# Performance work log

Measured on AMD Instinct MI355X. Metric: run time of the kernel, lower is better.

Reference implementation:

```python
import jax, jax.numpy as jnp
import numpy as np

B, P, E, D, A = 128, 49, 2048, 512, 512


def setup_inputs() -> dict:
    key = jax.random.key(0)
    ks = jax.random.split(key, 10)
    s = lambda k, shape, fan: jax.random.normal(k, shape, jnp.float32) * (1.0 / np.sqrt(fan))
    return {
        "encoder_out": jax.random.normal(ks[0], (B, P, E), jnp.float32),
        "decoder_hidden": jax.random.normal(ks[1], (B, D), jnp.float32),
        "We": s(ks[2], (A, E), E),  # encoder_att weight
        "be": jnp.zeros((A,), jnp.float32),
        "Wd": s(ks[3], (A, D), D),  # decoder_att weight
        "bd": jnp.zeros((A,), jnp.float32),
        "Wb": s(ks[4], (A, A, A), A),  # Bilinear weight [out,in1,in2]
        "bb": jnp.zeros((A,), jnp.float32),
        "Wf": s(ks[5], (1, A), A),  # full_att weight
        "bf": jnp.zeros((1,), jnp.float32),
    }


def reference(encoder_out, decoder_hidden, We, be, Wd, bd, Wb, bb, Wf, bf):
    # att1: [B,P,A]; att2: [B,A]
    att1 = jnp.einsum('bpe,ae->bpa', encoder_out, We) + be
    att2 = jnp.einsum('bd,ad->ba', decoder_hidden, Wd) + bd
    # nn.Bilinear(att1, att2_expanded): out[b,p,k] = sum_ij att1[b,p,i]*Wb[k,i,j]*att2[b,j] + bb[k]
    # contract att2 first since it is shared across the P=49 positions
    u = jnp.einsum('bj,kij->bki', att2, Wb)            # [B,A,A]
    bil = jnp.einsum('bpi,bki->bpk', att1, u) + bb     # [B,P,A]
    att = jnp.einsum('bpk,ok->bpo', jax.nn.relu(bil), Wf)[..., 0] + bf[0]  # [B,P]
    alpha = jax.nn.softmax(att, axis=1)                # [B,P]
    attention_weighted_encoding = jnp.einsum('bpe,bp->be', encoder_out, alpha)
    return (attention_weighted_encoding, alpha)
```

## Files before the change

### kernel.cpp

```cpp
#include <hip/hip_runtime.h>
#include <stdint.h>

typedef unsigned short ushort_t;
typedef float f32x4 __attribute__((ext_vector_type(4)));
typedef _Float16 half8 __attribute__((ext_vector_type(8)));
typedef ushort_t u16x4 __attribute__((ext_vector_type(4)));

#define DEVFN static __device__ __forceinline__

DEVFN ushort_t cvt_f16(float f) {
  union { _Float16 h; ushort_t u; } v;
  v.h = (_Float16)f;
  return v.u;
}

DEVFN half8 cvt_frag(f32x4 a, f32x4 b) {
  half8 r;
  r[0] = (_Float16)a[0]; r[1] = (_Float16)a[1];
  r[2] = (_Float16)a[2]; r[3] = (_Float16)a[3];
  r[4] = (_Float16)b[0]; r[5] = (_Float16)b[1];
  r[6] = (_Float16)b[2]; r[7] = (_Float16)b[3];
  return r;
}

DEVFN void gload16(const void* g, void* lds) {
  __builtin_amdgcn_global_load_lds(
      (const __attribute__((address_space(1))) uint32_t*)g,
      (__attribute__((address_space(3))) uint32_t*)lds, 16, 0, 0);
}

__global__ __launch_bounds__(256) void k_pre(
    const float* __restrict__ enc, const float* __restrict__ We,
    const float* __restrict__ dec, const float* __restrict__ Wd,
    const float* __restrict__ bd,
    ushort_t* __restrict__ encf16, ushort_t* __restrict__ Wef16,
    ushort_t* __restrict__ att2, float* __restrict__ att) {
  __shared__ __align__(16) float ds[512];
  const int bid = blockIdx.x, t = threadIdx.x;
  if (bid < 128) {
    int b = bid;
    ds[t] = dec[b * 512 + t];
    ds[t + 256] = dec[b * 512 + t + 256];
    __syncthreads();
    for (int o = 0; o < 2; ++o) {
      int a = o * 256 + t;
      const f32x4* wr = (const f32x4*)(Wd + (size_t)a * 512);
      const f32x4* dr = (const f32x4*)ds;
      f32x4 acc = {0.f, 0.f, 0.f, 0.f};
#pragma unroll 8
      for (int k4 = 0; k4 < 128; ++k4) acc += wr[k4] * dr[k4];
      float s = bd[a] + acc[0] + acc[1] + acc[2] + acc[3];
      att2[b * 512 + a] = cvt_f16(s);
    }
  } else if (bid == 128) {
    for (int i = t; i < 128 * 49; i += 256) att[i] = 0.f;
  } else {
    const int NQ_ENC = 3211264;
    const int NQ_TOT = 3473408;
    int idx = (bid - 129) * 256 + t;
    const int stride = 2048 * 256;
    for (int q = idx; q < NQ_TOT; q += stride) {
      const float* src; ushort_t* dst; int j;
      if (q < NQ_ENC) { src = enc; dst = encf16; j = q; }
      else            { src = We;  dst = Wef16;  j = q - NQ_ENC; }
      f32x4 v = ((const f32x4*)src)[j];
      u16x4 o;
      o[0] = cvt_f16(v[0]); o[1] = cvt_f16(v[1]);
      o[2] = cvt_f16(v[2]); o[3] = cvt_f16(v[3]);
      ((u16x4*)dst)[j] = o;
    }
  }
}

__global__ __launch_bounds__(256) void k_mm1(
    const ushort_t* __restrict__ Ae, const ushort_t* __restrict__ Be,
    const float* __restrict__ be,
    const ushort_t* __restrict__ att2, const float* __restrict__ Wb,
    ushort_t* __restrict__ att1, ushort_t* __restrict__ u) {
  __shared__ __align__(16) char smem[49152];
  const int bid = blockIdx.x;
  const int t = threadIdx.x, w = t >> 6, l = t & 63;
  const int wm = w >> 1, wn = w & 1;
  const int q = l >> 4, lm = l & 15;

  if (bid < 392) {
    ushort_t* As = (ushort_t*)smem;
    ushort_t* Bs = (ushort_t*)(smem + 8192);
    const int m0 = (bid >> 2) * 64, n0 = (bid & 3) * 128;
    f32x4 acc[2][4] = {};
    for (int ks = 0; ks < 32; ++ks) {
      const int k0 = ks * 64;
#pragma unroll
      for (int i = 0; i < 2; ++i) {
        int Lb = i * 256 + (w << 6);
        int L = Lb + l, r = L >> 3, s = L & 7, gc = s ^ (r & 7);
        gload16((const char*)(Ae + (size_t)(m0 + r) * 2048 + k0) + gc * 16,
                (char*)As + (size_t)Lb * 16);
      }
#pragma unroll
      for (int i = 0; i < 4; ++i) {
        int Lb = i * 256 + (w << 6);
        int L = Lb + l, r = L >> 3, s = L & 7, gc = s ^ (r & 7);
        gload16((const char*)(Be + (size_t)(n0 + r) * 2048 + k0) + gc * 16,
                (char*)Bs + (size_t)Lb * 16);
      }
      __syncthreads();
#pragma unroll
      for (int ksub = 0; ksub < 2; ++ksub) {
        half8 af[2], bfr[4];
#pragma unroll
        for (int mi = 0; mi < 2; ++mi) {
          int r = wm * 32 + mi * 16 + lm;
          int d = ksub * 4 + q;
          af[mi] = *(const half8*)((const char*)As + ((size_t)r * 8 + (d ^ (r & 7))) * 16);
        }
#pragma unroll
        for (int ni = 0; ni < 4; ++ni) {
          int r = wn * 64 + ni * 16 + lm;
          int d = ksub * 4 + q;
          bfr[ni] = *(const half8*)((const char*)Bs + ((size_t)r * 8 + (d ^ (r & 7))) * 16);
        }
#pragma unroll
        for (int mi = 0; mi < 2; ++mi)
#pragma unroll
          for (int ni = 0; ni < 4; ++ni)
            acc[mi][ni] = __builtin_amdgcn_mfma_f32_16x16x32_f16(af[mi], bfr[ni], acc[mi][ni], 0, 0, 0);
      }
      __syncthreads();
    }
    for (int mi = 0; mi < 2; ++mi)
      for (int ni = 0; ni < 4; ++ni)
        for (int rg = 0; rg < 4; ++rg) {
          int m = m0 + wm * 32 + mi * 16 + q * 4 + rg;
          int n = n0 + wn * 64 + ni * 16 + lm;
          att1[(size_t)m * 512 + n] = cvt_f16(acc[mi][ni][rg] + be[n]);
        }
  } else {
    ushort_t* As = (ushort_t*)smem;
    float*    Bs = (float*)(smem + 16384);
    const int n0 = (bid - 392) * 128;
    f32x4 acc[4][4] = {};
    for (int ks = 0; ks < 8; ++ks) {
      const int j0 = ks * 64;
#pragma unroll
      for (int i = 0; i < 4; ++i) {
        int Lb = i * 256 + (w << 6);
        int L = Lb + l, r = L >> 3, s = L & 7, gc = s ^ (r & 7);
        gload16((const char*)(att2 + (size_t)r * 512 + j0) + gc * 16,
                (char*)As + (size_t)Lb * 16);
      }
#pragma unroll
      for (int i = 0; i < 8; ++i) {
        int Lb = i * 256 + (w << 6);
        int L = Lb + l, r = L >> 4, s = L & 15, gc = s ^ (r & 15);
        gload16((const char*)(Wb + (size_t)(n0 + r) * 512 + j0) + gc * 16,
                (char*)Bs + (size_t)Lb * 16);
      }
      __syncthreads();
#pragma unroll
      for (int ksub = 0; ksub < 2; ++ksub) {
        half8 af[4], bfr[4];
#pragma unroll
        for (int mi = 0; mi < 4; ++mi) {
          int r = wm * 64 + mi * 16 + lm;
          int d = ksub * 4 + q;
          af[mi] = *(const half8*)((const char*)As + ((size_t)r * 8 + (d ^ (r & 7))) * 16);
        }
#pragma unroll
        for (int ni = 0; ni < 4; ++ni) {
          int r = wn * 64 + ni * 16 + lm;
          int d0 = ksub * 8 + q * 2;
          f32x4 v0 = *(const f32x4*)((const char*)Bs + ((size_t)r * 16 + (d0 ^ (r & 15))) * 16);
          f32x4 v1 = *(const f32x4*)((const char*)Bs + ((size_t)r * 16 + ((d0 + 1) ^ (r & 15))) * 16);
          bfr[ni] = cvt_frag(v0, v1);
        }
#pragma unroll
        for (int mi = 0; mi < 4; ++mi)
#pragma unroll
          for (int ni = 0; ni < 4; ++ni)
            acc[mi][ni] = __builtin_amdgcn_mfma_f32_16x16x32_f16(af[mi], bfr[ni], acc[mi][ni], 0, 0, 0);
      }
      __syncthreads();
    }
    for (int mi = 0; mi < 4; ++mi)
      for (int ni = 0; ni < 4; ++ni)
        for (int rg = 0; rg < 4; ++rg) {
          int b = wm * 64 + mi * 16 + q * 4 + rg;
          int n = n0 + wn * 64 + ni * 16 + lm;
          u[(size_t)b * 262144 + n] = cvt_f16(acc[mi][ni][rg]);
        }
  }
}

__global__ __launch_bounds__(256) void k_bil(
    const ushort_t* __restrict__ att1, const ushort_t* __restrict__ u,
    const float* __restrict__ bb, const float* __restrict__ Wf,
    float* __restrict__ att) {
  __shared__ __align__(16) ushort_t As[64 * 64];
  __shared__ __align__(16) ushort_t Bs[128 * 64];
  const int t = threadIdx.x, w = t >> 6, l = t & 63;
  const int wm = w >> 1, wn = w & 1;
  const int b = blockIdx.x, kq = blockIdx.y;
  const ushort_t* Arow = att1 + (size_t)b * 49 * 512;
  const ushort_t* Brow = u + (size_t)b * 262144 + (size_t)kq * 128 * 512;
  f32x4 acc[2][4] = {};
  for (int ks = 0; ks < 8; ++ks) {
    const int i0 = ks * 64;
#pragma unroll
    for (int i = 0; i < 2; ++i) {
      int Lb = i * 256 + (w << 6);
      int L = Lb + l, r = L >> 3, s = L & 7, gc = s ^ (r & 7);
      gload16((const char*)(Arow + (size_t)r * 512 + i0) + gc * 16,
              (char*)As + (size_t)Lb * 16);
    }
#pragma unroll
    for (int i = 0; i < 4; ++i) {
      int Lb = i * 256 + (w << 6);
      int L = Lb + l, r = L >> 3, s = L & 7, gc = s ^ (r & 7);
      gload16((const char*)(Brow + (size_t)r * 512 + i0) + gc * 16,
              (char*)Bs + (size_t)Lb * 16);
    }
    __syncthreads();
    const int q = l >> 4, lm = l & 15;
#pragma unroll
    for (int ksub = 0; ksub < 2; ++ksub) {
      half8 af[2], bfr[4];
#pragma unroll
      for (int mi = 0; mi < 2; ++mi) {
        int r = wm * 32 + mi * 16 + lm;
        int d = ksub * 4 + q;
        af[mi] = *(const half8*)((const char*)As + ((size_t)r * 8 + (d ^ (r & 7))) * 16);
      }
#pragma unroll
      for (int ni = 0; ni < 4; ++ni) {
        int r = wn * 64 + ni * 16 + lm;
        int d = ksub * 4 + q;
        bfr[ni] = *(const half8*)((const char*)Bs + ((size_t)r * 8 + (d ^ (r & 7))) * 16);
      }
#pragma unroll
      for (int mi = 0; mi < 2; ++mi)
#pragma unroll
        for (int ni = 0; ni < 4; ++ni)
          acc[mi][ni] = __builtin_amdgcn_mfma_f32_16x16x32_f16(af[mi], bfr[ni], acc[mi][ni], 0, 0, 0);
    }
    __syncthreads();
  }
  const int q = l >> 4, lm = l & 15;
#pragma unroll
  for (int mi = 0; mi < 2; ++mi) {
#pragma unroll
    for (int rg = 0; rg < 4; ++rg) {
      float s = 0.f;
#pragma unroll
      for (int ni = 0; ni < 4; ++ni) {
        int k = kq * 128 + wn * 64 + ni * 16 + lm;
        float v = acc[mi][ni][rg] + bb[k];
        s += fmaxf(v, 0.f) * Wf[k];
      }
      s += __shfl_xor(s, 1);
      s += __shfl_xor(s, 2);
      s += __shfl_xor(s, 4);
      s += __shfl_xor(s, 8);
      int p = wm * 32 + mi * 16 + q * 4 + rg;
      if (lm == 0 && p < 49) atomicAdd(att + b * 49 + p, s);
    }
  }
}

__global__ __launch_bounds__(256) void k_awe(
    const float* __restrict__ enc, const float* __restrict__ att,
    float* __restrict__ awe, float* __restrict__ alpha) {
  __shared__ float al[49];
  int b = blockIdx.y, h = blockIdx.x, t = threadIdx.x;
  if (t < 64) {
    float x = (t < 49) ? att[b * 49 + t] : -1e30f;
    float m = x;
    for (int off = 32; off; off >>= 1) m = fmaxf(m, __shfl_xor(m, off));
    float e = (t < 49) ? __expf(x - m) : 0.f;
    float s = e;
    for (int off = 32; off; off >>= 1) s += __shfl_xor(s, off);
    if (t < 49) {
      float a = e / s;
      al[t] = a;
      if (h == 0) alpha[b * 49 + t] = a;
    }
  }
  __syncthreads();
  int e4 = h * 256 + t;
  const f32x4* ep = (const f32x4*)(enc + (size_t)b * 49 * 2048) + e4;
  f32x4 acc = {0.f, 0.f, 0.f, 0.f};
#pragma unroll 7
  for (int p = 0; p < 49; ++p) acc += al[p] * ep[(size_t)p * 512];
  ((f32x4*)(awe + (size_t)b * 2048))[e4] = acc;
}

extern "C" void kernel_launch(void* const* d_in, const int* in_sizes, int n_in,
                              void* d_out, int out_size, void* d_ws, size_t ws_size,
                              hipStream_t stream) {
  (void)in_sizes; (void)n_in; (void)out_size; (void)ws_size;
  const float* enc = (const float*)d_in[0];
  const float* dec = (const float*)d_in[1];
  const float* We  = (const float*)d_in[2];
  const float* be  = (const float*)d_in[3];
  const float* Wd  = (const float*)d_in[4];
  const float* bd  = (const float*)d_in[5];
  const float* Wb  = (const float*)d_in[6];
  const float* bb  = (const float*)d_in[7];
  const float* Wf  = (const float*)d_in[8];

  char* ws = (char*)d_ws;
  ushort_t* att2   = (ushort_t*)ws;
  ushort_t* att1   = (ushort_t*)(ws + 131072);
  ushort_t* u      = (ushort_t*)(ws + 6619136);
  float*    att    = (float*)(ws + 73728000);
  ushort_t* encf16 = (ushort_t*)(ws + 73753088);
  ushort_t* Wef16  = (ushort_t*)(ws + 99443200);

  float* awe   = (float*)d_out;
  float* alpha = (float*)d_out + 262144;

  k_pre<<<dim3(2177), 256, 0, stream>>>(enc, We, dec, Wd, bd, encf16, Wef16, att2, att);
  k_mm1<<<dim3(2440), 256, 0, stream>>>(encf16, Wef16, be, att2, Wb, att1, u);
  k_bil<<<dim3(128, 4), 256, 0, stream>>>(att1, u, bb, Wf, att);
  k_awe<<<dim3(2, 128), 256, 0, stream>>>(enc, att, awe, alpha);
}
```

Before: 799.1 us.

## Fuse fp32-to-fp16 conversion of encoder and We into the matmul tile loads

Drops the separate pass that turned encoder_out and We into fp16 buffers. The att1 matmul now copies fp32 tiles straight into shared memory, using a 16-chunk XOR swizzle, and converts to fp16 fragments just before the MFMA. This removes one full read and write of the encoder tensor, at the cost of twice the shared-memory traffic per tile and extra conversion work in the inner loop, with We tiles converted again by every block. The final weighted-sum kernel also switches to 128 threads and twice as many blocks.

```diff
diff --git a/kernel.cpp b/kernel.cpp
--- a/kernel.cpp
+++ b/kernel.cpp
@@ -30,10 +30,8 @@
 }
 
 __global__ __launch_bounds__(256) void k_pre(
-    const float* __restrict__ enc, const float* __restrict__ We,
     const float* __restrict__ dec, const float* __restrict__ Wd,
     const float* __restrict__ bd,
-    ushort_t* __restrict__ encf16, ushort_t* __restrict__ Wef16,
     ushort_t* __restrict__ att2, float* __restrict__ att) {
   __shared__ __align__(16) float ds[512];
   const int bid = blockIdx.x, t = threadIdx.x;
@@ -52,28 +50,13 @@
       float s = bd[a] + acc[0] + acc[1] + acc[2] + acc[3];
       att2[b * 512 + a] = cvt_f16(s);
     }
-  } else if (bid == 128) {
+  } else {
     for (int i = t; i < 128 * 49; i += 256) att[i] = 0.f;
-  } else {
-    const int NQ_ENC = 3211264;
-    const int NQ_TOT = 3473408;
-    int idx = (bid - 129) * 256 + t;
-    const int stride = 2048 * 256;
-    for (int q = idx; q < NQ_TOT; q += stride) {
-      const float* src; ushort_t* dst; int j;
-      if (q < NQ_ENC) { src = enc; dst = encf16; j = q; }
-      else            { src = We;  dst = Wef16;  j = q - NQ_ENC; }
-      f32x4 v = ((const f32x4*)src)[j];
-      u16x4 o;
-      o[0] = cvt_f16(v[0]); o[1] = cvt_f16(v[1]);
-      o[2] = cvt_f16(v[2]); o[3] = cvt_f16(v[3]);
-      ((u16x4*)dst)[j] = o;
-    }
   }
 }
 
 __global__ __launch_bounds__(256) void k_mm1(
-    const ushort_t* __restrict__ Ae, const ushort_t* __restrict__ Be,
+    const float* __restrict__ Ae, const float* __restrict__ Be,
     const float* __restrict__ be,
     const ushort_t* __restrict__ att2, const float* __restrict__ Wb,
     ushort_t* __restrict__ att1, ushort_t* __restrict__ u) {
@@ -84,23 +67,23 @@
   const int q = l >> 4, lm = l & 15;
 
   if (bid < 392) {
-    ushort_t* As = (ushort_t*)smem;
-    ushort_t* Bs = (ushort_t*)(smem + 8192);
+    float* As = (float*)smem;
+    float* Bs = (float*)(smem + 16384);
     const int m0 = (bid >> 2) * 64, n0 = (bid & 3) * 128;
     f32x4 acc[2][4] = {};
     for (int ks = 0; ks < 32; ++ks) {
       const int k0 = ks * 64;
 #pragma unroll
-      for (int i = 0; i < 2; ++i) {
+      for (int i = 0; i < 4; ++i) {
         int Lb = i * 256 + (w << 6);
-        int L = Lb + l, r = L >> 3, s = L & 7, gc = s ^ (r & 7);
+        int L = Lb + l, r = L >> 4, s = L & 15, gc = s ^ (r & 15);
         gload16((const char*)(Ae + (size_t)(m0 + r) * 2048 + k0) + gc * 16,
                 (char*)As + (size_t)Lb * 16);
       }
 #pragma unroll
-      for (int i = 0; i < 4; ++i) {
+      for (int i = 0; i < 8; ++i) {
         int Lb = i * 256 + (w << 6);
-        int L = Lb + l, r = L >> 3, s = L & 7, gc = s ^ (r & 7);
+        int L = Lb + l, r = L >> 4, s = L & 15, gc = s ^ (r & 15);
         gload16((const char*)(Be + (size_t)(n0 + r) * 2048 + k0) + gc * 16,
                 (char*)Bs + (size_t)Lb * 16);
       }
@@ -111,14 +94,18 @@
 #pragma unroll
         for (int mi = 0; mi < 2; ++mi) {
           int r = wm * 32 + mi * 16 + lm;
-          int d = ksub * 4 + q;
-          af[mi] = *(const half8*)((const char*)As + ((size_t)r * 8 + (d ^ (r & 7))) * 16);
+          int d0 = ksub * 8 + q * 2;
+          f32x4 v0 = *(const f32x4*)((const char*)As + ((size_t)r * 16 + (d0 ^ (r & 15))) * 16);
+          f32x4 v1 = *(const f32x4*)((const char*)As + ((size_t)r * 16 + ((d0 + 1) ^ (r & 15))) * 16);
+          af[mi] = cvt_frag(v0, v1);
         }
 #pragma unroll
         for (int ni = 0; ni < 4; ++ni) {
           int r = wn * 64 + ni * 16 + lm;
-          int d = ksub * 4 + q;
-          bfr[ni] = *(const half8*)((const char*)Bs + ((size_t)r * 8 + (d ^ (r & 7))) * 16);
+          int d0 = ksub * 8 + q * 2;
+          f32x4 v0 = *(const f32x4*)((const char*)Bs + ((size_t)r * 16 + (d0 ^ (r & 15))) * 16);
+          f32x4 v1 = *(const f32x4*)((const char*)Bs + ((size_t)r * 16 + ((d0 + 1) ^ (r & 15))) * 16);
+          bfr[ni] = cvt_frag(v0, v1);
         }
 #pragma unroll
         for (int mi = 0; mi < 2; ++mi)
@@ -267,7 +254,7 @@
   }
 }
 
-__global__ __launch_bounds__(256) void k_awe(
+__global__ __launch_bounds__(128) void k_awe(
     const float* __restrict__ enc, const float* __restrict__ att,
     float* __restrict__ awe, float* __restrict__ alpha) {
   __shared__ float al[49];
@@ -286,7 +273,7 @@
     }
   }
   __syncthreads();
-  int e4 = h * 256 + t;
+  int e4 = h * 128 + t;
   const f32x4* ep = (const f32x4*)(enc + (size_t)b * 49 * 2048) + e4;
   f32x4 acc = {0.f, 0.f, 0.f, 0.f};
 #pragma unroll 7
@@ -313,14 +300,12 @@
   ushort_t* att1   = (ushort_t*)(ws + 131072);
   ushort_t* u      = (ushort_t*)(ws + 6619136);
   float*    att    = (float*)(ws + 73728000);
-  ushort_t* encf16 = (ushort_t*)(ws + 73753088);
-  ushort_t* Wef16  = (ushort_t*)(ws + 99443200);
 
   float* awe   = (float*)d_out;
   float* alpha = (float*)d_out + 262144;
 
-  k_pre<<<dim3(2177), 256, 0, stream>>>(enc, We, dec, Wd, bd, encf16, Wef16, att2, att);
-  k_mm1<<<dim3(2440), 256, 0, stream>>>(encf16, Wef16, be, att2, Wb, att1, u);
+  k_pre<<<dim3(129), 256, 0, stream>>>(dec, Wd, bd, att2, att);
+  k_mm1<<<dim3(2440), 256, 0, stream>>>(enc, We, be, att2, Wb, att1, u);
   k_bil<<<dim3(128, 4), 256, 0, stream>>>(att1, u, bb, Wf, att);
-  k_awe<<<dim3(2, 128), 256, 0, stream>>>(enc, att, awe, alpha);
-}
+  k_awe<<<dim3(4, 128), 128, 0, stream>>>(enc, att, awe, alpha);
+}
```

New measurement: 816.0 us. 2.1% more time.
